# Kernel optimization log

Hardware: AMD Instinct MI355X
Metric: run time of the kernel (lower is better)

Reference implementation:

```python
import jax, jax.numpy as jnp
import numpy as np
from jax import lax

NPOINTS = 1024
K = 32
EPS = 1e-5


def fps(xyz, npoints):
    # Furthest point sampling. xyz: (B, N, 3) -> idx (B, npoints) int32.
    B, N, _ = xyz.shape
    def step(carry, _):
        dists, last = carry
        last_xyz = jnp.take_along_axis(xyz, last[:, None, None], axis=1)  # (B,1,3)
        d = jnp.sum((xyz - last_xyz) ** 2, axis=-1)  # (B,N)
        dists = jnp.minimum(dists, d)
        nxt = jnp.argmax(dists, axis=-1).astype(jnp.int32)
        return (dists, nxt), last
    init = (jnp.full((B, N), 1e10, xyz.dtype), jnp.zeros((B,), jnp.int32))
    _, idx = lax.scan(step, init, None, length=npoints)
    return idx.T  # (B, npoints)


def knn_idx(new_xyz, xyz, k):
    # new_xyz (B,S,3), xyz (B,N,3) -> (B,S,k) indices of k nearest neighbors.
    d = (jnp.sum(new_xyz ** 2, -1)[:, :, None]
         - 2.0 * jnp.einsum('bsc,bnc->bsn', new_xyz, xyz)
         + jnp.sum(xyz ** 2, -1)[:, None, :])  # (B,S,N)
    _, idx = lax.top_k(-d, k)
    return idx


def batch_gather(x, idx):
    # x (B, N, C), idx (B, ...) -> (B, ..., C)
    return jax.vmap(lambda a, i: a[i])(x, idx)


def bn(x, g, b, axes):
    # training-mode batchnorm over `axes`, channel on last axis
    m = jnp.mean(x, axes, keepdims=True)
    v = jnp.var(x, axes, keepdims=True)
    return g * (x - m) * lax.rsqrt(v + EPS) + b


def setup_inputs() -> dict:
    key = jax.random.key(0)
    ks = jax.random.split(key, 8)
    B, N, D, Cw, OUT = 16, 4096, 64, 64, 64
    inp = {
        'xyz': jax.random.uniform(ks[0], (B, N, 3), jnp.float32),
        'feature': jax.random.normal(ks[1], (B, D, N), jnp.float32),
        'w0': jax.random.normal(ks[2], (3, Cw), jnp.float32) * 0.3,
        'b0': jnp.zeros((Cw,), jnp.float32),
        'g0': jnp.ones((Cw,), jnp.float32),
        'be0': jnp.zeros((Cw,), jnp.float32),
        'w1': jax.random.normal(ks[3], (Cw, Cw), jnp.float32) * 0.1,
        'b1': jnp.zeros((Cw,), jnp.float32),
        'g1': jnp.ones((Cw,), jnp.float32),
        'be1': jnp.zeros((Cw,), jnp.float32),
        'w2': jax.random.normal(ks[4], (Cw, Cw), jnp.float32) * 0.1,
        'b2': jnp.zeros((Cw,), jnp.float32),
        'g2': jnp.ones((Cw,), jnp.float32),
        'be2': jnp.zeros((Cw,), jnp.float32),
        'wf': jax.random.normal(ks[5], (D * Cw, OUT), jnp.float32) * 0.02,
        'bf': jnp.zeros((OUT,), jnp.float32),
        'gf': jnp.ones((OUT,), jnp.float32),
        'bef': jnp.zeros((OUT,), jnp.float32),
    }
    return inp


def reference(xyz, feature, w0, b0, g0, be0, w1, b1, g1, be1, w2, b2, g2, be2, wf, bf, gf, bef):
    B, N, _ = xyz.shape
    # FPS + gather centroids
    fps_idx = fps(xyz, NPOINTS)                    # (B, S)
    new_xyz = batch_gather(xyz, fps_idx)           # (B, S, 3)
    # kNN grouping
    idx = knn_idx(new_xyz, xyz, K)                 # (B, S, K)
    grouped_xyz = batch_gather(xyz, idx) - new_xyz[:, :, None, :]   # (B,S,K,3)
    feat_nlast = jnp.swapaxes(feature, 1, 2)       # (B, N, D)
    grouped_feature = batch_gather(feat_nlast, idx)  # (B, S, K, D)
    # WeightNet: 1x1 conv MLP 3 -> Cw -> Cw -> Cw with BN+ReLU
    h = grouped_xyz
    for w, b, g, be in ((w0, b0, g0, be0), (w1, b1, g1, be1), (w2, b2, g2, be2)):
        h = jax.nn.relu(bn(h @ w + b, g, be, (0, 1, 2)))  # (B,S,K,Cw)
    weights = h
    # per-centroid matmul: (B,S,D,K) x (B,S,K,Cw) -> (B,S,D,Cw)
    nf = jnp.einsum('bskd,bskw->bsdw', grouped_feature, weights)
    nf = nf.reshape(B, NPOINTS, -1)                # (B, S, D*Cw)
    # final Conv1d(1x1) + BN1d + ReLU
    out = jax.nn.relu(bn(nf @ wf + bf, gf, bef, (0, 1)))  # (B, S, OUT)
    out = jnp.swapaxes(out, 1, 2)                  # (B, OUT, S)
    return (new_xyz, out)
```

## Files before the change

kernel.cpp:

```cpp
#include <hip/hip_runtime.h>

#define NBATCH 16
#define NPTS   4096
#define NSAMP  1024
#define NKNN   32
#define NROWS  (NBATCH*NSAMP*NKNN)
#define BN_EPS 1e-5f
#define H1PAD  66
#define KNN_CAP 512

typedef __attribute__((ext_vector_type(4))) float f32x4;
typedef __attribute__((ext_vector_type(8))) short bf16x8;
union frag_u { unsigned u[4]; bf16x8 h; uint4 u4; };

__device__ __forceinline__ unsigned pack_bf16pair(float a, float b) {
    unsigned ua = __float_as_uint(a); ua += 0x7FFFu + ((ua >> 16) & 1u);
    unsigned ub = __float_as_uint(b); ub += 0x7FFFu + ((ub >> 16) & 1u);
    return (ua >> 16) | (ub & 0xFFFF0000u);
}
__device__ __forceinline__ unsigned short bf16_rne(float a) {
    unsigned ua = __float_as_uint(a); ua += 0x7FFFu + ((ua >> 16) & 1u);
    return (unsigned short)(ua >> 16);
}

__global__ __launch_bounds__(256) void fps_kernel(const float* __restrict__ xyz,
                                                  float* __restrict__ newxyz)
{
    const int b = blockIdx.x;
    const int tid = threadIdx.x;
    const int wv = tid >> 6;
    const float* xb = xyz + (size_t)b * NPTS * 3;
    __shared__ float xs[NPTS];
    __shared__ float ys[NPTS];
    __shared__ float zs[NPTS];
    __shared__ __align__(16) float4 red[2][4];
    __shared__ __align__(16) float nxs[NSAMP*3];
    float px[16], py[16], pz[16], dmin[16];
    {
        float arr[48];
        const float4* s4 = (const float4*)(xb + (size_t)tid * 48);
        #pragma unroll
        for (int i = 0; i < 12; ++i) *(float4*)&arr[i*4] = s4[i];
        #pragma unroll
        for (int j = 0; j < 16; ++j) {
            px[j] = arr[3*j]; py[j] = arr[3*j+1]; pz[j] = arr[3*j+2];
            const int p = tid * 16 + j;
            xs[p] = px[j]; ys[p] = py[j]; zs[p] = pz[j];
            dmin[j] = 1e10f;
        }
    }
    if (tid == 0) { nxs[0] = xb[0]; nxs[1] = xb[1]; nxs[2] = xb[2]; }
    __syncthreads();
    float lx = xs[0], ly = ys[0], lz = zs[0];
    for (int t = 1; t < NSAMP; ++t) {
        float bv = -1.0f;
        #pragma unroll
        for (int j = 0; j < 16; ++j) {
            const float dx = __fsub_rn(px[j], lx);
            const float dy = __fsub_rn(py[j], ly);
            const float dz = __fsub_rn(pz[j], lz);
            const float d = __fadd_rn(__fadd_rn(__fmul_rn(dx,dx), __fmul_rn(dy,dy)), __fmul_rn(dz,dz));
            const float nd = fminf(dmin[j], d);
            dmin[j] = nd;
            bv = fmaxf(bv, nd);
        }
        int lj = 0;
        #pragma unroll
        for (int j = 15; j >= 0; --j) if (dmin[j] == bv) lj = j;
        const int bi_lane = tid * 16 + lj;
        float mv = bv;
        {
            int s_;
            s_ = __builtin_amdgcn_mov_dpp(__float_as_int(mv), 0x111, 0xf, 0xf, true);
            mv = fmaxf(mv, __int_as_float(s_));
            s_ = __builtin_amdgcn_mov_dpp(__float_as_int(mv), 0x112, 0xf, 0xf, true);
            mv = fmaxf(mv, __int_as_float(s_));
            s_ = __builtin_amdgcn_mov_dpp(__float_as_int(mv), 0x114, 0xf, 0xf, true);
            mv = fmaxf(mv, __int_as_float(s_));
            s_ = __builtin_amdgcn_mov_dpp(__float_as_int(mv), 0x118, 0xf, 0xf, true);
            mv = fmaxf(mv, __int_as_float(s_));
            s_ = __builtin_amdgcn_mov_dpp(__float_as_int(mv), 0x142, 0xf, 0xf, true);
            mv = fmaxf(mv, __int_as_float(s_));
            s_ = __builtin_amdgcn_mov_dpp(__float_as_int(mv), 0x143, 0xf, 0xf, true);
            mv = fmaxf(mv, __int_as_float(s_));
        }
        mv = __int_as_float(__builtin_amdgcn_readlane(__float_as_int(mv), 63));
        const unsigned long long mask = __ballot(bv == mv);
        const int winner = __ffsll(mask) - 1;
        const int bi_w = __builtin_amdgcn_readlane(bi_lane, winner);
        const float wx = xs[bi_w], wy = ys[bi_w], wz = zs[bi_w];
        const int par = t & 1;
        if ((tid & 63) == 0) red[par][wv] = make_float4(mv, wx, wy, wz);
        __syncthreads();
        float4 w0 = red[par][0];
        const float4 w1 = red[par][1];
        const float4 w2 = red[par][2];
        const float4 w3 = red[par][3];
        if (w1.x > w0.x) w0 = w1;
        if (w2.x > w0.x) w0 = w2;
        if (w3.x > w0.x) w0 = w3;
        lx = w0.y; ly = w0.z; lz = w0.w;
        if (tid == 0) { nxs[t*3] = lx; nxs[t*3+1] = ly; nxs[t*3+2] = lz; }
    }
    __syncthreads();
    {
        float4* d4 = (float4*)(newxyz + (size_t)b * NSAMP * 3);
        const float4* s4 = (const float4*)nxs;
        #pragma unroll
        for (int i = tid; i < NSAMP*3/4; i += 256) d4[i] = s4[i];
    }
}

__device__ __forceinline__ void bin_select(int* hist, int* ctrl, int* wsum,
                                           int tid, int shift)
{
    const int lane = tid & 63, wv = tid >> 6;
    const int cnt = hist[tid];
    const int r = ctrl[1];
    int incl = cnt;
    #pragma unroll
    for (int d = 1; d < 64; d <<= 1) {
        const int v = __shfl_up(incl, d);
        if (lane >= d) incl += v;
    }
    if (lane == 63) wsum[wv] = incl;
    __syncthreads();
    int base = 0;
    if (wv > 0) base += wsum[0];
    if (wv > 1) base += wsum[1];
    if (wv > 2) base += wsum[2];
    incl += base;
    const int excl = incl - cnt;
    if (excl < r && r <= incl) {
        ctrl[0] |= tid << shift;
        ctrl[1] = r - excl;
        ctrl[2] = cnt;
    }
}

__global__ __launch_bounds__(256) void knn_kernel(const float* __restrict__ xyz,
                                                  const float* __restrict__ newxyz,
                                                  int* __restrict__ idx_out)
{
    const int bs = blockIdx.x;
    const int b = bs >> 10;
    const int tid = threadIdx.x;
    const int lane = tid & 63;
    __shared__ unsigned keys[NPTS];
    __shared__ int hist[256];
    __shared__ float qsh[3];
    __shared__ int ctrl[8];
    __shared__ int wsum[4];
    __shared__ int cl[KNN_CAP];
    __shared__ int lt[32];
    __shared__ int ties[128];
    if (tid < 3) qsh[tid] = newxyz[bs*3 + tid];
    if (tid == 0) { ctrl[0] = 0; ctrl[1] = NKNN; }
    hist[tid] = 0;
    __syncthreads();
    const float q0 = qsh[0], q1 = qsh[1], q2 = qsh[2];
    const float qq = __fadd_rn(__fadd_rn(__fmul_rn(q0,q0), __fmul_rn(q1,q1)), __fmul_rn(q2,q2));
    const float* xb = xyz + (size_t)b * NPTS * 3;
    for (int n = tid; n < NPTS; n += 256) {
        const float x0 = xb[n*3+0], x1 = xb[n*3+1], x2 = xb[n*3+2];
        const float xx = __fadd_rn(__fadd_rn(__fmul_rn(x0,x0), __fmul_rn(x1,x1)), __fmul_rn(x2,x2));
        float dt = __fmul_rn(q0, x0);
        dt = __fmaf_rn(q1, x1, dt);
        dt = __fmaf_rn(q2, x2, dt);
        const float dd = __fadd_rn(__fsub_rn(qq, __fmul_rn(2.0f, dt)), xx);
        unsigned ub = __float_as_uint(dd);
        ub = (ub & 0x80000000u) ? ~ub : (ub | 0x80000000u);
        keys[n] = ub;
        const int bin = (int)(ub >> 24);
        unsigned long long act = __ballot(true);
        while (act) {
            const int leader = __ffsll(act) - 1;
            const int lbin = __builtin_amdgcn_readlane(bin, leader);
            const unsigned long long same = __ballot(bin == lbin);
            if (lane == leader) atomicAdd(&hist[lbin], (int)__popcll(same));
            act &= ~same;
        }
    }
    __syncthreads();
    bin_select(hist, ctrl, wsum, tid, 24);
    __syncthreads();
    const unsigned pf3 = (unsigned)ctrl[0];
    const int bin3 = (int)(pf3 >> 24);
    const int m = ctrl[2];
    const bool compact = (m <= KNN_CAP);
    if (tid == 0) { ctrl[3] = 0; ctrl[4] = 0; ctrl[5] = 0; ctrl[6] = 0; }
    __syncthreads();
    if (compact) {
        for (int n = tid; n < NPTS; n += 256) {
            const int tb = (int)(keys[n] >> 24);
            if (tb == bin3)      { const int pos = atomicAdd(&ctrl[3], 1); cl[pos] = n; }
            else if (tb < bin3)  { const int pos = atomicAdd(&ctrl[4], 1); lt[pos] = n; }
        }
    }
    __syncthreads();
    for (int p = 2; p >= 0; --p) {
        hist[tid] = 0;
        __syncthreads();
        const unsigned pre = (unsigned)ctrl[0];
        const int shift = p * 8;
        const unsigned himask = 0xFFFFFFFFu << ((p + 1) * 8);
        if (compact) {
            const int eqn = ctrl[3];
            for (int i = tid; i < eqn; i += 256) {
                const unsigned k = keys[cl[i]];
                if ((k & himask) == pre) atomicAdd(&hist[(k >> shift) & 255], 1);
            }
        } else {
            for (int n = tid; n < NPTS; n += 256) {
                const unsigned k = keys[n];
                if ((k & himask) == pre) atomicAdd(&hist[(k >> shift) & 255], 1);
            }
        }
        __syncthreads();
        bin_select(hist, ctrl, wsum, tid, shift);
        __syncthreads();
    }
    const unsigned T = (unsigned)ctrl[0];
    int* out = idx_out + (size_t)bs * NKNN;
    if (compact) {
        const int ltn = ctrl[4];
        if (tid == 0) ctrl[5] = ltn;
        __syncthreads();
        if (tid < ltn) out[tid] = lt[tid];
        const int eqn = ctrl[3];
        for (int i = tid; i < eqn; i += 256) {
            const int n = cl[i];
            const unsigned k = keys[n];
            if (k < T) {
                const int pos = atomicAdd(&ctrl[5], 1);
                if (pos < NKNN) out[pos] = n;
            } else if (k == T) {
                const int pos = atomicAdd(&ctrl[6], 1);
                if (pos < 128) ties[pos] = n;
            }
        }
    } else {
        for (int n = tid; n < NPTS; n += 256) {
            const unsigned k = keys[n];
            if (k < T) {
                const int pos = atomicAdd(&ctrl[5], 1);
                if (pos < NKNN) out[pos] = n;
            } else if (k == T) {
                const int pos = atomicAdd(&ctrl[6], 1);
                if (pos < 128) ties[pos] = n;
            }
        }
    }
    __syncthreads();
    if (tid == 0) {
        const int nless = ctrl[5] < NKNN ? ctrl[5] : NKNN;
        const int need = NKNN - nless;
        const int ntie = ctrl[6] < 128 ? ctrl[6] : 128;
        int last = -1;
        for (int j = 0; j < need; ++j) {
            int best = 0x7fffffff;
            for (int i = 0; i < ntie; ++i) {
                const int v = ties[i];
                if (v > last && v < best) best = v;
            }
            out[nless + j] = (best == 0x7fffffff) ? 0 : best;
            last = best;
        }
    }
}

__global__ __launch_bounds__(256) void feat_transpose_kernel(
    const float* __restrict__ feat, unsigned short* __restrict__ tfeat)
{
    __shared__ unsigned short t[64][65];
    const int blk = blockIdx.x;
    const int b = blk >> 6, nt = blk & 63;
    const int tid = threadIdx.x;
    #pragma unroll
    for (int i = 0; i < 16; ++i) {
        const int e = i*256 + tid;
        const int d = e >> 6, n = e & 63;
        t[n][d] = bf16_rne(feat[((size_t)(b*64 + d))*NPTS + nt*64 + n]);
    }
    __syncthreads();
    #pragma unroll
    for (int i = 0; i < 16; ++i) {
        const int e = i*256 + tid;
        const int n = e >> 6, d = e & 63;
        tfeat[((size_t)(b*NPTS) + nt*64 + n)*64 + d] = t[n][d];
    }
}

__global__ void zero_all_kernel(double* st, float* g1, float* g2)
{
    const int i = blockIdx.x * 256 + threadIdx.x;
    if (i < 512) st[i] = 0.0;
    if (i < 4096) { g1[i] = 0.f; g2[i] = 0.f; }
}

__global__ __launch_bounds__(256) void gxmoments_kernel(
    const float* __restrict__ xyz, const float* __restrict__ newxyz,
    const int* __restrict__ idxws, double* __restrict__ stats,
    float* __restrict__ gxws)
{
    const int tid = threadIdx.x;
    float m[9];
    #pragma unroll
    for (int i = 0; i < 9; ++i) m[i] = 0.f;
    for (int row = blockIdx.x * 256 + tid; row < NROWS; row += gridDim.x * 256) {
        const int bs = row >> 5;
        const int bb = row >> 15;
        const int id = idxws[row];
        const float* xp = xyz + ((size_t)bb * NPTS + id) * 3;
        const float* qp = newxyz + bs * 3;
        const float dx = xp[0] - qp[0];
        const float dy = xp[1] - qp[1];
        const float dz = xp[2] - qp[2];
        gxws[(size_t)row*3 + 0] = dx;
        gxws[(size_t)row*3 + 1] = dy;
        gxws[(size_t)row*3 + 2] = dz;
        m[0] += dx; m[1] += dy; m[2] += dz;
        m[3] += dx*dx; m[4] += dx*dy; m[5] += dx*dz;
        m[6] += dy*dy; m[7] += dy*dz; m[8] += dz*dz;
    }
    double d[9];
    #pragma unroll
    for (int i = 0; i < 9; ++i) {
        d[i] = (double)m[i];
        #pragma unroll
        for (int s = 1; s < 64; s <<= 1) d[i] += __shfl_xor(d[i], s);
    }
    __shared__ double part[4][9];
    if ((tid & 63) == 0) {
        #pragma unroll
        for (int i = 0; i < 9; ++i) part[tid >> 6][i] = d[i];
    }
    __syncthreads();
    if (tid < 9) atomicAdd(&stats[tid], part[0][tid] + part[1][tid] + part[2][tid] + part[3][tid]);
}

__global__ void bn0_moments_finalize_kernel(const double* __restrict__ st,
    const float* __restrict__ w0, const float* __restrict__ b0,
    const float* __restrict__ g0, const float* __restrict__ be0,
    float* __restrict__ outp)
{
    const int c = threadIdx.x;
    const double N = (double)NROWS;
    const double w0c = w0[c], w1c = w0[64 + c], w2c = w0[128 + c];
    const double b = b0[c];
    const double dotS = st[0]*w0c + st[1]*w1c + st[2]*w2c;
    const double qf = w0c*w0c*st[3] + w1c*w1c*st[6] + w2c*w2c*st[8]
                    + 2.0*(w0c*w1c*st[4] + w0c*w2c*st[5] + w1c*w2c*st[7]);
    const double mean = dotS / N + b;
    const double ex2 = (qf + 2.0*b*dotS) / N + b*b;
    const double var = ex2 - mean*mean;
    const float scale = g0[c] * rsqrtf((float)var + BN_EPS);
    outp[c] = scale;
    outp[64 + c] = be0[c] - (float)mean * scale;
}

__global__ void wfpack_all_kernel(const float* __restrict__ wf,
                                  const float* __restrict__ w1,
                                  const float* __restrict__ w2,
                                  unsigned* __restrict__ wfb,
                                  unsigned* __restrict__ w1b,
                                  unsigned* __restrict__ w2b)
{
    int blk = blockIdx.x;
    const float* src; unsigned* dst;
    if (blk < 512)      { src = wf; dst = wfb; }
    else if (blk < 520) { src = w1; dst = w1b; blk -= 512; }
    else                { src = w2; dst = w2b; blk -= 520; }
    const int kt = blk >> 2, ot = blk & 3;
    const int l = threadIdx.x;
    const int o = ot*16 + (l & 15);
    const int kb = kt*32 + (l >> 4)*8;
    unsigned out[4];
    #pragma unroll
    for (int r = 0; r < 4; ++r) {
        const float a = src[(size_t)(kb + 2*r) * 64 + o];
        const float b = src[(size_t)(kb + 2*r + 1) * 64 + o];
        out[r] = pack_bf16pair(a, b);
    }
    *(uint4*)&dst[((size_t)blk * 64 + l) * 4] = *(const uint4*)out;
}

__global__ __launch_bounds__(256) void gram1_kernel(
    const float* __restrict__ gxws,
    const float* __restrict__ w0, const float* __restrict__ b0,
    const float* __restrict__ bnp, float* __restrict__ G1,
    double* __restrict__ Sh1)
{
    __shared__ float gxs[32][3];
    __shared__ float h1s[32][H1PAD];
    __shared__ float rsum[256];
    const int tid = threadIdx.x;
    const int c = tid & 63;
    const int rq = tid >> 6;
    const int lg = c >> 4, lm = c & 15;
    const float w0c0 = w0[c], w0c1 = w0[64+c], w0c2 = w0[128+c];
    const float b0c = b0[c], sc0 = bnp[c], sh0 = bnp[64+c];
    f32x4 Ga[4] = {{0,0,0,0},{0,0,0,0},{0,0,0,0},{0,0,0,0}};
    float sumh = 0.f;
    for (int chunk = blockIdx.x; chunk < NROWS/32; chunk += gridDim.x) {
        if (tid < 96) ((float*)gxs)[tid] = gxws[(size_t)chunk*96 + tid];
        __syncthreads();
        #pragma unroll
        for (int i = 0; i < 8; ++i) {
            const int r = rq*8 + i;
            const float t0 = gxs[r][0]*w0c0 + gxs[r][1]*w0c1 + gxs[r][2]*w0c2 + b0c;
            const float h = fmaxf(sc0*t0 + sh0, 0.f);
            h1s[r][c] = h;
            sumh += h;
        }
        __syncthreads();
        frag_u fr[4];
        #pragma unroll
        for (int ct = 0; ct < 4; ++ct)
            #pragma unroll
            for (int r = 0; r < 4; ++r)
                fr[ct].u[r] = pack_bf16pair(h1s[lg*8 + 2*r][ct*16 + lm],
                                            h1s[lg*8 + 2*r + 1][ct*16 + lm]);
        #pragma unroll
        for (int ct = 0; ct < 4; ++ct)
            Ga[ct] = __builtin_amdgcn_mfma_f32_16x16x32_bf16(fr[rq].h, fr[ct].h, Ga[ct], 0, 0, 0);
        __syncthreads();
    }
    #pragma unroll
    for (int ct = 0; ct < 4; ++ct)
        #pragma unroll
        for (int r = 0; r < 4; ++r)
            atomicAdd(&G1[(rq*16 + lg*4 + r)*64 + ct*16 + lm], Ga[ct][r]);
    rsum[tid] = sumh;
    __syncthreads();
    if (tid < 64) atomicAdd(&Sh1[c], (double)(rsum[c] + rsum[64+c] + rsum[128+c] + rsum[192+c]));
}

__global__ __launch_bounds__(256) void gram2_kernel(
    const float* __restrict__ gxws,
    const float* __restrict__ w0, const float* __restrict__ b0,
    const float* __restrict__ b1, const unsigned* __restrict__ w1b,
    const float* __restrict__ bnp, float* __restrict__ G2,
    double* __restrict__ Sh2)
{
    __shared__ float gxs[32][3];
    __shared__ float h1s[32][H1PAD];
    __shared__ float h2s[32][H1PAD];
    __shared__ float rsum[256];
    const int tid = threadIdx.x;
    const int c = tid & 63;
    const int rq = tid >> 6;
    const int lg = c >> 4, lm = c & 15;
    const int c2 = rq*16 + lm;
    const float w0c0 = w0[c], w0c1 = w0[64+c], w0c2 = w0[128+c];
    const float b0c = b0[c], sc0 = bnp[c], sh0 = bnp[64+c];
    const float b1c2 = b1[c2], sc1 = bnp[128+c2], sh1 = bnp[192+c2];
    frag_u Bw1[2];
    Bw1[0].u4 = *(const uint4*)&w1b[((0*4 + rq)*64 + c)*4];
    Bw1[1].u4 = *(const uint4*)&w1b[((1*4 + rq)*64 + c)*4];
    f32x4 Ga[4] = {{0,0,0,0},{0,0,0,0},{0,0,0,0},{0,0,0,0}};
    float sumh = 0.f;
    for (int chunk = blockIdx.x; chunk < NROWS/32; chunk += gridDim.x) {
        if (tid < 96) ((float*)gxs)[tid] = gxws[(size_t)chunk*96 + tid];
        __syncthreads();
        #pragma unroll
        for (int i = 0; i < 8; ++i) {
            const int r = rq*8 + i;
            const float t0 = gxs[r][0]*w0c0 + gxs[r][1]*w0c1 + gxs[r][2]*w0c2 + b0c;
            h1s[r][c] = fmaxf(sc0*t0 + sh0, 0.f);
        }
        __syncthreads();
        #pragma unroll
        for (int mt = 0; mt < 2; ++mt) {
            f32x4 acc = {0,0,0,0};
            #pragma unroll
            for (int kt = 0; kt < 2; ++kt) {
                frag_u a;
                #pragma unroll
                for (int r = 0; r < 4; ++r) {
                    const float2 f = *(const float2*)&h1s[mt*16 + lm][kt*32 + lg*8 + 2*r];
                    a.u[r] = pack_bf16pair(f.x, f.y);
                }
                acc = __builtin_amdgcn_mfma_f32_16x16x32_bf16(a.h, Bw1[kt].h, acc, 0, 0, 0);
            }
            #pragma unroll
            for (int r = 0; r < 4; ++r)
                h2s[mt*16 + lg*4 + r][c2] = fmaxf(sc1*(acc[r] + b1c2) + sh1, 0.f);
        }
        __syncthreads();
        #pragma unroll
        for (int i = 0; i < 8; ++i) sumh += h2s[rq*8 + i][c];
        frag_u fr[4];
        #pragma unroll
        for (int ct = 0; ct < 4; ++ct)
            #pragma unroll
            for (int r = 0; r < 4; ++r)
                fr[ct].u[r] = pack_bf16pair(h2s[lg*8 + 2*r][ct*16 + lm],
                                            h2s[lg*8 + 2*r + 1][ct*16 + lm]);
        #pragma unroll
        for (int ct = 0; ct < 4; ++ct)
            Ga[ct] = __builtin_amdgcn_mfma_f32_16x16x32_bf16(fr[rq].h, fr[ct].h, Ga[ct], 0, 0, 0);
        __syncthreads();
    }
    #pragma unroll
    for (int ct = 0; ct < 4; ++ct)
        #pragma unroll
        for (int r = 0; r < 4; ++r)
            atomicAdd(&G2[(rq*16 + lg*4 + r)*64 + ct*16 + lm], Ga[ct][r]);
    rsum[tid] = sumh;
    __syncthreads();
    if (tid < 64) atomicAdd(&Sh2[c], (double)(rsum[c] + rsum[64+c] + rsum[128+c] + rsum[192+c]));
}

__global__ __launch_bounds__(256) void bn_gram_finalize_kernel(
    const double* __restrict__ Sh, const float* __restrict__ G,
    const float* __restrict__ w, const float* __restrict__ bias,
    const float* __restrict__ g, const float* __restrict__ be,
    float* __restrict__ outp)
{
    __shared__ float wls[64][65];
    __shared__ double shl[64];
    __shared__ double rd[256], rqd[256];
    const int tid = threadIdx.x;
    const int c = tid & 63;
    const int rqi = tid >> 6;
    for (int i = tid; i < 4096; i += 256) wls[i >> 6][i & 63] = w[i];
    if (tid < 64) shl[tid] = Sh[tid];
    __syncthreads();
    double dot = 0.0, quad = 0.0;
    for (int j = rqi*16; j < rqi*16 + 16; ++j) {
        const double wjc = (double)wls[j][c];
        dot += wjc * shl[j];
        double inner = 0.0;
        for (int k = 0; k < 64; ++k) inner += (double)G[j*64 + k] * (double)wls[k][c];
        quad += wjc * inner;
    }
    rd[tid] = dot; rqd[tid] = quad;
    __syncthreads();
    if (tid < 64) {
        const double d = rd[c] + rd[64+c] + rd[128+c] + rd[192+c];
        const double q = rqd[c] + rqd[64+c] + rqd[128+c] + rqd[192+c];
        const double N = (double)NROWS;
        const double bc = (double)bias[c];
        const double mean = d / N + bc;
        const double ex2 = (q + 2.0*bc*d) / N + bc*bc;
        const double var = ex2 - mean*mean;
        const float scale = g[c] * rsqrtf((float)var + BN_EPS);
        outp[c] = scale;
        outp[64 + c] = be[c] - (float)mean * scale;
    }
}

__global__ void bn_finalize_kernel(const double* __restrict__ st,
                                   const float* __restrict__ g,
                                   const float* __restrict__ be,
                                   float* __restrict__ outp, float n)
{
    const int c = threadIdx.x;
    const double m = st[c] / (double)n;
    const double var = st[64 + c] / (double)n - m * m;
    const float scale = g[c] * rsqrtf((float)var + BN_EPS);
    outp[c] = scale;
    outp[64 + c] = be[c] - (float)m * scale;
}

__global__ __launch_bounds__(256) void final_conv_kernel(
    const float* __restrict__ gxws,
    const int* __restrict__ idxws, const unsigned short* __restrict__ tfeat,
    const float* __restrict__ w0, const float* __restrict__ b0,
    const float* __restrict__ b1, const float* __restrict__ b2,
    const float* __restrict__ bnp, const unsigned* __restrict__ wfb,
    const unsigned* __restrict__ w1b, const unsigned* __restrict__ w2b,
    const float* __restrict__ bf, float* __restrict__ y)
{
    __shared__ unsigned wtp[8][16][64];
    __shared__ __align__(16) float scratch[2*64*H1PAD];
    __shared__ float gxs[256][3];
    __shared__ int   idxs[8][32];
    float* h1s = scratch;
    float* h2s = scratch + 64*H1PAD;
    unsigned* yaf = (unsigned*)scratch;
    const int tid = threadIdx.x;
    const int c = tid & 63;
    const int rq = tid >> 6;
    const int lg = c >> 4, lm = c & 15;
    const int c2 = rq*16 + lm;
    const int bs0 = blockIdx.x * 8;
    const int b = bs0 >> 10;
    idxs[tid >> 5][tid & 31] = idxws[(size_t)bs0 * NKNN + tid];
    const float w0c0 = w0[c], w0c1 = w0[64+c], w0c2 = w0[128+c];
    const float b0c = b0[c], sc0 = bnp[c], sh0 = bnp[64+c];
    const float b1c2 = b1[c2], sc1 = bnp[128+c2], sh1 = bnp[192+c2];
    const float b2c2 = b2[c2], sc2 = bnp[256+c2], sh2 = bnp[320+c2];
    frag_u Bw1[2], Bw2[2];
    #pragma unroll
    for (int kt = 0; kt < 2; ++kt) {
        Bw1[kt].u4 = *(const uint4*)&w1b[((kt*4 + rq)*64 + c)*4];
        Bw2[kt].u4 = *(const uint4*)&w2b[((kt*4 + rq)*64 + c)*4];
    }
    for (int i = tid; i < 768; i += 256)
        ((float*)gxs)[i] = gxws[(size_t)bs0*96 + i];
    __syncthreads();
    for (int chunk = 0; chunk < 4; ++chunk) {
        #pragma unroll
        for (int i = 0; i < 16; ++i) {
            const int r = rq*16 + i;
            const int gr = chunk*64 + r;
            const float t0 = gxs[gr][0]*w0c0 + gxs[gr][1]*w0c1 + gxs[gr][2]*w0c2 + b0c;
            h1s[r*H1PAD + c] = fmaxf(sc0*t0 + sh0, 0.f);
        }
        __syncthreads();
        #pragma unroll
        for (int mt = 0; mt < 4; ++mt) {
            f32x4 acc = {0,0,0,0};
            #pragma unroll
            for (int kt = 0; kt < 2; ++kt) {
                frag_u a;
                #pragma unroll
                for (int r = 0; r < 4; ++r) {
                    const float2 f = *(const float2*)&h1s[(mt*16 + lm)*H1PAD + kt*32 + lg*8 + 2*r];
                    a.u[r] = pack_bf16pair(f.x, f.y);
                }
                acc = __builtin_amdgcn_mfma_f32_16x16x32_bf16(a.h, Bw1[kt].h, acc, 0, 0, 0);
            }
            #pragma unroll
            for (int r = 0; r < 4; ++r)
                h2s[(mt*16 + lg*4 + r)*H1PAD + c2] = fmaxf(sc1*(acc[r] + b1c2) + sh1, 0.f);
        }
        __syncthreads();
        #pragma unroll
        for (int mt = 0; mt < 4; ++mt) {
            f32x4 acc = {0,0,0,0};
            #pragma unroll
            for (int kt = 0; kt < 2; ++kt) {
                frag_u a;
                #pragma unroll
                for (int r = 0; r < 4; ++r) {
                    const float2 f = *(const float2*)&h2s[(mt*16 + lm)*H1PAD + kt*32 + lg*8 + 2*r];
                    a.u[r] = pack_bf16pair(f.x, f.y);
                }
                acc = __builtin_amdgcn_mfma_f32_16x16x32_bf16(a.h, Bw2[kt].h, acc, 0, 0, 0);
            }
            float wt[4];
            #pragma unroll
            for (int r = 0; r < 4; ++r)
                wt[r] = fmaxf(sc2*(acc[r] + b2c2) + sh2, 0.f);
            const int grow0 = chunk*64 + mt*16 + lg*4;
            const int e = grow0 >> 5, kl = grow0 & 31;
            wtp[e][kl >> 1][c2]       = pack_bf16pair(wt[0], wt[1]);
            wtp[e][(kl >> 1) + 1][c2] = pack_bf16pair(wt[2], wt[3]);
        }
        __syncthreads();
    }
    const int lane = c;
    const int wid = rq;
    frag_u afr[2][4];
    #pragma unroll
    for (int es = 0; es < 2; ++es)
        #pragma unroll
        for (int w4 = 0; w4 < 4; ++w4)
            #pragma unroll
            for (int r = 0; r < 4; ++r)
                afr[es][w4].u[r] = wtp[wid*2 + es][lg*4 + r][w4*16 + lm];
    f32x4 yaccA = {0.f, 0.f, 0.f, 0.f};
    f32x4 yaccB = {0.f, 0.f, 0.f, 0.f};
    const unsigned short* tfb = tfeat + (size_t)b * NPTS * 64;
    for (int dhalf = 0; dhalf < 2; ++dhalf) {
        #pragma unroll
        for (int es = 0; es < 2; ++es) {
            const int e = wid*2 + es;
            #pragma unroll
            for (int dt = 0; dt < 2; ++dt) {
                const int d = dhalf*32 + dt*16 + lm;
                frag_u B;
                #pragma unroll
                for (int r = 0; r < 4; ++r) {
                    const int k0 = lg*8 + 2*r;
                    const unsigned va = tfb[(size_t)idxs[e][k0]   * 64 + d];
                    const unsigned vb = tfb[(size_t)idxs[e][k0+1] * 64 + d];
                    B.u[r] = va | (vb << 16);
                }
                #pragma unroll
                for (int w4 = 0; w4 < 4; ++w4) {
                    f32x4 dnf = {0.f, 0.f, 0.f, 0.f};
                    dnf = __builtin_amdgcn_mfma_f32_16x16x32_bf16(afr[es][w4].h, B.h, dnf, 0, 0, 0);
                    const unsigned p0 = pack_bf16pair(dnf[0], dnf[1]);
                    const unsigned p1 = pack_bf16pair(dnf[2], dnf[3]);
                    const int dloc = dt*16 + lm;
                    const int kp0 = dloc*32 + w4*8 + lg*2;
                    const int sw = kp0 ^ ((lm & 3) << 3) ^ ((e & 7) << 2);
                    *(uint2*)&yaf[e*1024 + sw] = make_uint2(p0, p1);
                }
            }
        }
        __syncthreads();
        for (int kt = 0; kt < 64; kt += 2) {
            frag_u A0, B0, A1, B1;
            const int kpb0 = (kt*16 + lg*4) ^ (((kt >> 1) & 3) << 3) ^ ((lm & 7) << 2);
            const int kpb1 = ((kt+1)*16 + lg*4) ^ ((((kt+1) >> 1) & 3) << 3) ^ ((lm & 7) << 2);
            A0.u4 = *(const uint4*)&yaf[(lm & 7)*1024 + kpb0];
            A1.u4 = *(const uint4*)&yaf[(lm & 7)*1024 + kpb1];
            B0.u4 = *(const uint4*)&wfb[(((size_t)(dhalf*64 + kt)*4 + wid)*64 + lane)*4];
            B1.u4 = *(const uint4*)&wfb[(((size_t)(dhalf*64 + kt + 1)*4 + wid)*64 + lane)*4];
            yaccA = __builtin_amdgcn_mfma_f32_16x16x32_bf16(A0.h, B0.h, yaccA, 0, 0, 0);
            yaccB = __builtin_amdgcn_mfma_f32_16x16x32_bf16(A1.h, B1.h, yaccB, 0, 0, 0);
        }
        __syncthreads();
    }
    if (lg < 2) {
        const float bfo = bf[wid*16 + lm];
        #pragma unroll
        for (int r = 0; r < 4; ++r)
            y[(size_t)(bs0 + lg*4 + r) * 64 + wid*16 + lm] = (yaccA[r] + yaccB[r]) + bfo;
    }
}

__global__ __launch_bounds__(256) void ystats_kernel(const float* __restrict__ y,
                                                     double* __restrict__ st)
{
    const int tid = threadIdx.x;
    const int c = tid & 63;
    double s = 0.0, s2 = 0.0;
    for (int i = blockIdx.x * 256 + tid; i < NBATCH*NSAMP*64; i += gridDim.x * 256) {
        const float v = y[i];
        s += v; s2 += (double)v * (double)v;
    }
    __shared__ double rs[256], rs2[256];
    rs[tid] = s; rs2[tid] = s2;
    __syncthreads();
    if (tid < 64) {
        const double a  = rs[c]  + rs[64+c]  + rs[128+c]  + rs[192+c];
        const double a2 = rs2[c] + rs2[64+c] + rs2[128+c] + rs2[192+c];
        atomicAdd(&st[c], a);
        atomicAdd(&st[64 + c], a2);
    }
}

__global__ void writeout_kernel(const float* __restrict__ y,
                                const float* __restrict__ bnp3,
                                float* __restrict__ outp)
{
    const int i = blockIdx.x * 256 + threadIdx.x;
    if (i >= NBATCH * 64 * NSAMP) return;
    const int s = i & 1023;
    const int o = (i >> 10) & 63;
    const int bb = i >> 16;
    const float v = y[((size_t)(bb << 10) + s) * 64 + o];
    outp[i] = fmaxf(bnp3[o] * v + bnp3[64 + o], 0.f);
}

extern "C" void kernel_launch(void* const* d_in, const int* in_sizes, int n_in,
                              void* d_out, int out_size, void* d_ws, size_t ws_size,
                              hipStream_t stream)
{
    (void)in_sizes; (void)n_in; (void)out_size; (void)ws_size;
    const float* xyz  = (const float*)d_in[0];
    const float* feat = (const float*)d_in[1];
    const float* w0   = (const float*)d_in[2];
    const float* b0   = (const float*)d_in[3];
    const float* g0   = (const float*)d_in[4];
    const float* be0  = (const float*)d_in[5];
    const float* w1   = (const float*)d_in[6];
    const float* b1   = (const float*)d_in[7];
    const float* g1   = (const float*)d_in[8];
    const float* be1  = (const float*)d_in[9];
    const float* w2   = (const float*)d_in[10];
    const float* b2   = (const float*)d_in[11];
    const float* g2   = (const float*)d_in[12];
    const float* be2  = (const float*)d_in[13];
    const float* wf   = (const float*)d_in[14];
    const float* bf   = (const float*)d_in[15];
    const float* gf   = (const float*)d_in[16];
    const float* bef  = (const float*)d_in[17];

    float* out = (float*)d_out;
    float* newxyz = out;
    float* outmain = out + NBATCH * NSAMP * 3;

    char* ws = (char*)d_ws;
    int*      idxws = (int*)ws;
    float*    ybuf  = (float*)(ws + 2097152);
    double*   stats = (double*)(ws + 6291456);
    float*    bnp   = (float*)(ws + 6295552);
    unsigned* wfb   = (unsigned*)(ws + 6297600);
    unsigned* w1b   = (unsigned*)(ws + 6821888);
    unsigned* w2b   = (unsigned*)(ws + 6830080);
    float*    G1    = (float*)(ws + 6838272);
    float*    G2    = (float*)(ws + 6854656);
    float*    gxws  = (float*)(ws + 6871040);
    unsigned short* tfeat = (unsigned short*)(ws + 13164544);

    zero_all_kernel<<<16, 256, 0, stream>>>(stats, G1, G2);
    wfpack_all_kernel<<<528, 64, 0, stream>>>(wf, w1, w2, wfb, w1b, w2b);
    feat_transpose_kernel<<<1024, 256, 0, stream>>>(feat, tfeat);
    fps_kernel<<<NBATCH, 256, 0, stream>>>(xyz, newxyz);
    knn_kernel<<<NBATCH * NSAMP, 256, 0, stream>>>(xyz, newxyz, idxws);

    gxmoments_kernel<<<1024, 256, 0, stream>>>(xyz, newxyz, idxws, stats, gxws);
    bn0_moments_finalize_kernel<<<1, 64, 0, stream>>>(stats, w0, b0, g0, be0, bnp);
    gram1_kernel<<<256, 256, 0, stream>>>(gxws, w0, b0, bnp, G1, stats + 128);
    bn_gram_finalize_kernel<<<1, 256, 0, stream>>>(stats + 128, G1, w1, b1, g1, be1, bnp + 128);
    gram2_kernel<<<256, 256, 0, stream>>>(gxws, w0, b0, b1, w1b, bnp, G2, stats + 192);
    bn_gram_finalize_kernel<<<1, 256, 0, stream>>>(stats + 192, G2, w2, b2, g2, be2, bnp + 256);

    final_conv_kernel<<<NBATCH * NSAMP / 8, 256, 0, stream>>>(
        gxws, idxws, tfeat, w0, b0, b1, b2, bnp, wfb, w1b, w2b, bf, ybuf);

    ystats_kernel<<<256, 256, 0, stream>>>(ybuf, stats + 384);
    bn_finalize_kernel<<<1, 64, 0, stream>>>(stats + 384, gf, bef, bnp + 384, (float)(NBATCH * NSAMP));
    writeout_kernel<<<4096, 256, 0, stream>>>(ybuf, bnp + 384, outmain);
}
```

Measured before the change: 1.236 ms.

## Merge FPS, transpose, weight packing and zeroing into one prep launch; fuse grouped-xyz into kNN

The zero, weight-pack and feature-transpose kernels are folded into the FPS launch as extra blocks, sharing LDS through a union. The aim is to overlap the serial 16-block FPS with the independent prep work and to cut launch count. The kNN kernel now stages its indices in LDS and writes the centered neighbour coordinates itself, so gxmoments only reads gxws instead of gathering. The risk is that the larger LDS footprint of the merged kernel limits occupancy for the transpose blocks.

```diff
diff --git a/kernel.cpp b/kernel.cpp
--- a/kernel.cpp
+++ b/kernel.cpp
@@ -23,18 +23,74 @@
     return (unsigned short)(ua >> 16);
 }
 
-__global__ __launch_bounds__(256) void fps_kernel(const float* __restrict__ xyz,
-                                                  float* __restrict__ newxyz)
-{
-    const int b = blockIdx.x;
+union PrepLds {
+    struct {
+        float xs[NPTS]; float ys[NPTS]; float zs[NPTS];
+        float4 red[2][4];
+        float nxs[NSAMP*3];
+    } f;
+    unsigned short tt[64][65];
+};
+
+__global__ __launch_bounds__(256) void prep_kernel(
+    const float* __restrict__ xyz, float* __restrict__ newxyz,
+    const float* __restrict__ feat, unsigned short* __restrict__ tfeat,
+    const float* __restrict__ wf, const float* __restrict__ w1,
+    const float* __restrict__ w2, unsigned* __restrict__ wfb,
+    unsigned* __restrict__ w1b, unsigned* __restrict__ w2b,
+    double* __restrict__ st, float* __restrict__ g1f, float* __restrict__ g2f)
+{
+    __shared__ PrepLds L;
+    const int blk = blockIdx.x;
     const int tid = threadIdx.x;
+    if (blk >= 1172) {
+        const int i = (blk - 1172) * 256 + tid;
+        if (i < 512) st[i] = 0.0;
+        if (i < 4096) { g1f[i] = 0.f; g2f[i] = 0.f; }
+        return;
+    }
+    if (blk >= 1040) {
+        const int unit = (blk - 1040) * 4 + (tid >> 6);
+        const int l = tid & 63;
+        int u = unit;
+        const float* src; unsigned* dst;
+        if (u < 512)      { src = wf; dst = wfb; }
+        else if (u < 520) { src = w1; dst = w1b; u -= 512; }
+        else              { src = w2; dst = w2b; u -= 520; }
+        const int kt = u >> 2, ot = u & 3;
+        const int o = ot*16 + (l & 15);
+        const int kb = kt*32 + (l >> 4)*8;
+        unsigned outp[4];
+        #pragma unroll
+        for (int r = 0; r < 4; ++r) {
+            const float a = src[(size_t)(kb + 2*r) * 64 + o];
+            const float b = src[(size_t)(kb + 2*r + 1) * 64 + o];
+            outp[r] = pack_bf16pair(a, b);
+        }
+        *(uint4*)&dst[((size_t)u * 64 + l) * 4] = *(const uint4*)outp;
+        return;
+    }
+    if (blk >= 16) {
+        const int t = blk - 16;
+        const int b = t >> 6, nt = t & 63;
+        #pragma unroll
+        for (int i = 0; i < 16; ++i) {
+            const int e = i*256 + tid;
+            const int d = e >> 6, n = e & 63;
+            L.tt[n][d] = bf16_rne(feat[((size_t)(b*64 + d))*NPTS + nt*64 + n]);
+        }
+        __syncthreads();
+        #pragma unroll
+        for (int i = 0; i < 16; ++i) {
+            const int e = i*256 + tid;
+            const int n = e >> 6, d = e & 63;
+            tfeat[((size_t)(b*NPTS) + nt*64 + n)*64 + d] = L.tt[n][d];
+        }
+        return;
+    }
+    const int b = blk;
     const int wv = tid >> 6;
     const float* xb = xyz + (size_t)b * NPTS * 3;
-    __shared__ float xs[NPTS];
-    __shared__ float ys[NPTS];
-    __shared__ float zs[NPTS];
-    __shared__ __align__(16) float4 red[2][4];
-    __shared__ __align__(16) float nxs[NSAMP*3];
     float px[16], py[16], pz[16], dmin[16];
     {
         float arr[48];
@@ -45,13 +101,13 @@
         for (int j = 0; j < 16; ++j) {
             px[j] = arr[3*j]; py[j] = arr[3*j+1]; pz[j] = arr[3*j+2];
             const int p = tid * 16 + j;
-            xs[p] = px[j]; ys[p] = py[j]; zs[p] = pz[j];
+            L.f.xs[p] = px[j]; L.f.ys[p] = py[j]; L.f.zs[p] = pz[j];
             dmin[j] = 1e10f;
         }
     }
-    if (tid == 0) { nxs[0] = xb[0]; nxs[1] = xb[1]; nxs[2] = xb[2]; }
-    __syncthreads();
-    float lx = xs[0], ly = ys[0], lz = zs[0];
+    if (tid == 0) { L.f.nxs[0] = xb[0]; L.f.nxs[1] = xb[1]; L.f.nxs[2] = xb[2]; }
+    __syncthreads();
+    float lx = L.f.xs[0], ly = L.f.ys[0], lz = L.f.zs[0];
     for (int t = 1; t < NSAMP; ++t) {
         float bv = -1.0f;
         #pragma unroll
@@ -88,24 +144,24 @@
         const unsigned long long mask = __ballot(bv == mv);
         const int winner = __ffsll(mask) - 1;
         const int bi_w = __builtin_amdgcn_readlane(bi_lane, winner);
-        const float wx = xs[bi_w], wy = ys[bi_w], wz = zs[bi_w];
+        const float wx = L.f.xs[bi_w], wy = L.f.ys[bi_w], wz = L.f.zs[bi_w];
         const int par = t & 1;
-        if ((tid & 63) == 0) red[par][wv] = make_float4(mv, wx, wy, wz);
-        __syncthreads();
-        float4 w0 = red[par][0];
-        const float4 w1 = red[par][1];
-        const float4 w2 = red[par][2];
-        const float4 w3 = red[par][3];
-        if (w1.x > w0.x) w0 = w1;
-        if (w2.x > w0.x) w0 = w2;
-        if (w3.x > w0.x) w0 = w3;
+        if ((tid & 63) == 0) L.f.red[par][wv] = make_float4(mv, wx, wy, wz);
+        __syncthreads();
+        float4 w0 = L.f.red[par][0];
+        const float4 w1v = L.f.red[par][1];
+        const float4 w2v = L.f.red[par][2];
+        const float4 w3v = L.f.red[par][3];
+        if (w1v.x > w0.x) w0 = w1v;
+        if (w2v.x > w0.x) w0 = w2v;
+        if (w3v.x > w0.x) w0 = w3v;
         lx = w0.y; ly = w0.z; lz = w0.w;
-        if (tid == 0) { nxs[t*3] = lx; nxs[t*3+1] = ly; nxs[t*3+2] = lz; }
+        if (tid == 0) { L.f.nxs[t*3] = lx; L.f.nxs[t*3+1] = ly; L.f.nxs[t*3+2] = lz; }
     }
     __syncthreads();
     {
         float4* d4 = (float4*)(newxyz + (size_t)b * NSAMP * 3);
-        const float4* s4 = (const float4*)nxs;
+        const float4* s4 = (const float4*)L.f.nxs;
         #pragma unroll
         for (int i = tid; i < NSAMP*3/4; i += 256) d4[i] = s4[i];
     }
@@ -140,7 +196,8 @@
 
 __global__ __launch_bounds__(256) void knn_kernel(const float* __restrict__ xyz,
                                                   const float* __restrict__ newxyz,
-                                                  int* __restrict__ idx_out)
+                                                  int* __restrict__ idx_out,
+                                                  float* __restrict__ gxws)
 {
     const int bs = blockIdx.x;
     const int b = bs >> 10;
@@ -154,6 +211,7 @@
     __shared__ int cl[KNN_CAP];
     __shared__ int lt[32];
     __shared__ int ties[128];
+    __shared__ int outl[NKNN];
     if (tid < 3) qsh[tid] = newxyz[bs*3 + tid];
     if (tid == 0) { ctrl[0] = 0; ctrl[1] = NKNN; }
     hist[tid] = 0;
@@ -221,19 +279,18 @@
         __syncthreads();
     }
     const unsigned T = (unsigned)ctrl[0];
-    int* out = idx_out + (size_t)bs * NKNN;
     if (compact) {
         const int ltn = ctrl[4];
         if (tid == 0) ctrl[5] = ltn;
         __syncthreads();
-        if (tid < ltn) out[tid] = lt[tid];
+        if (tid < ltn) outl[tid] = lt[tid];
         const int eqn = ctrl[3];
         for (int i = tid; i < eqn; i += 256) {
             const int n = cl[i];
             const unsigned k = keys[n];
             if (k < T) {
                 const int pos = atomicAdd(&ctrl[5], 1);
-                if (pos < NKNN) out[pos] = n;
+                if (pos < NKNN) outl[pos] = n;
             } else if (k == T) {
                 const int pos = atomicAdd(&ctrl[6], 1);
                 if (pos < 128) ties[pos] = n;
@@ -244,7 +301,7 @@
             const unsigned k = keys[n];
             if (k < T) {
                 const int pos = atomicAdd(&ctrl[5], 1);
-                if (pos < NKNN) out[pos] = n;
+                if (pos < NKNN) outl[pos] = n;
             } else if (k == T) {
                 const int pos = atomicAdd(&ctrl[6], 1);
                 if (pos < 128) ties[pos] = n;
@@ -263,62 +320,29 @@
                 const int v = ties[i];
                 if (v > last && v < best) best = v;
             }
-            out[nless + j] = (best == 0x7fffffff) ? 0 : best;
+            outl[nless + j] = (best == 0x7fffffff) ? 0 : best;
             last = best;
         }
     }
-}
-
-__global__ __launch_bounds__(256) void feat_transpose_kernel(
-    const float* __restrict__ feat, unsigned short* __restrict__ tfeat)
-{
-    __shared__ unsigned short t[64][65];
-    const int blk = blockIdx.x;
-    const int b = blk >> 6, nt = blk & 63;
-    const int tid = threadIdx.x;
-    #pragma unroll
-    for (int i = 0; i < 16; ++i) {
-        const int e = i*256 + tid;
-        const int d = e >> 6, n = e & 63;
-        t[n][d] = bf16_rne(feat[((size_t)(b*64 + d))*NPTS + nt*64 + n]);
-    }
-    __syncthreads();
-    #pragma unroll
-    for (int i = 0; i < 16; ++i) {
-        const int e = i*256 + tid;
-        const int n = e >> 6, d = e & 63;
-        tfeat[((size_t)(b*NPTS) + nt*64 + n)*64 + d] = t[n][d];
-    }
-}
-
-__global__ void zero_all_kernel(double* st, float* g1, float* g2)
-{
-    const int i = blockIdx.x * 256 + threadIdx.x;
-    if (i < 512) st[i] = 0.0;
-    if (i < 4096) { g1[i] = 0.f; g2[i] = 0.f; }
+    __syncthreads();
+    if (tid < NKNN) idx_out[(size_t)bs * NKNN + tid] = outl[tid];
+    if (tid < 96) {
+        const int k = tid / 3, cc = tid % 3;
+        gxws[((size_t)bs * NKNN + k) * 3 + cc] = xb[outl[k]*3 + cc] - qsh[cc];
+    }
 }
 
 __global__ __launch_bounds__(256) void gxmoments_kernel(
-    const float* __restrict__ xyz, const float* __restrict__ newxyz,
-    const int* __restrict__ idxws, double* __restrict__ stats,
-    float* __restrict__ gxws)
+    const float* __restrict__ gxws, double* __restrict__ stats)
 {
     const int tid = threadIdx.x;
     float m[9];
     #pragma unroll
     for (int i = 0; i < 9; ++i) m[i] = 0.f;
     for (int row = blockIdx.x * 256 + tid; row < NROWS; row += gridDim.x * 256) {
-        const int bs = row >> 5;
-        const int bb = row >> 15;
-        const int id = idxws[row];
-        const float* xp = xyz + ((size_t)bb * NPTS + id) * 3;
-        const float* qp = newxyz + bs * 3;
-        const float dx = xp[0] - qp[0];
-        const float dy = xp[1] - qp[1];
-        const float dz = xp[2] - qp[2];
-        gxws[(size_t)row*3 + 0] = dx;
-        gxws[(size_t)row*3 + 1] = dy;
-        gxws[(size_t)row*3 + 2] = dz;
+        const float dx = gxws[(size_t)row*3 + 0];
+        const float dy = gxws[(size_t)row*3 + 1];
+        const float dz = gxws[(size_t)row*3 + 2];
         m[0] += dx; m[1] += dy; m[2] += dz;
         m[3] += dx*dx; m[4] += dx*dy; m[5] += dx*dz;
         m[6] += dy*dy; m[7] += dy*dz; m[8] += dz*dz;
@@ -357,32 +381,6 @@
     const float scale = g0[c] * rsqrtf((float)var + BN_EPS);
     outp[c] = scale;
     outp[64 + c] = be0[c] - (float)mean * scale;
-}
-
-__global__ void wfpack_all_kernel(const float* __restrict__ wf,
-                                  const float* __restrict__ w1,
-                                  const float* __restrict__ w2,
-                                  unsigned* __restrict__ wfb,
-                                  unsigned* __restrict__ w1b,
-                                  unsigned* __restrict__ w2b)
-{
-    int blk = blockIdx.x;
-    const float* src; unsigned* dst;
-    if (blk < 512)      { src = wf; dst = wfb; }
-    else if (blk < 520) { src = w1; dst = w1b; blk -= 512; }
-    else                { src = w2; dst = w2b; blk -= 520; }
-    const int kt = blk >> 2, ot = blk & 3;
-    const int l = threadIdx.x;
-    const int o = ot*16 + (l & 15);
-    const int kb = kt*32 + (l >> 4)*8;
-    unsigned out[4];
-    #pragma unroll
-    for (int r = 0; r < 4; ++r) {
-        const float a = src[(size_t)(kb + 2*r) * 64 + o];
-        const float b = src[(size_t)(kb + 2*r + 1) * 64 + o];
-        out[r] = pack_bf16pair(a, b);
-    }
-    *(uint4*)&dst[((size_t)blk * 64 + l) * 4] = *(const uint4*)out;
 }
 
 __global__ __launch_bounds__(256) void gram1_kernel(
@@ -790,13 +788,12 @@
     float*    gxws  = (float*)(ws + 6871040);
     unsigned short* tfeat = (unsigned short*)(ws + 13164544);
 
-    zero_all_kernel<<<16, 256, 0, stream>>>(stats, G1, G2);
-    wfpack_all_kernel<<<528, 64, 0, stream>>>(wf, w1, w2, wfb, w1b, w2b);
-    feat_transpose_kernel<<<1024, 256, 0, stream>>>(feat, tfeat);
-    fps_kernel<<<NBATCH, 256, 0, stream>>>(xyz, newxyz);
-    knn_kernel<<<NBATCH * NSAMP, 256, 0, stream>>>(xyz, newxyz, idxws);
-
-    gxmoments_kernel<<<1024, 256, 0, stream>>>(xyz, newxyz, idxws, stats, gxws);
+    prep_kernel<<<1188, 256, 0, stream>>>(xyz, newxyz, feat, tfeat,
+                                          wf, w1, w2, wfb, w1b, w2b,
+                                          stats, G1, G2);
+    knn_kernel<<<NBATCH * NSAMP, 256, 0, stream>>>(xyz, newxyz, idxws, gxws);
+
+    gxmoments_kernel<<<1024, 256, 0, stream>>>(gxws, stats);
     bn0_moments_finalize_kernel<<<1, 64, 0, stream>>>(stats, w0, b0, g0, be0, bnp);
     gram1_kernel<<<256, 256, 0, stream>>>(gxws, w0, b0, bnp, G1, stats + 128);
     bn_gram_finalize_kernel<<<1, 256, 0, stream>>>(stats + 128, G1, w1, b1, g1, be1, bnp + 128);
```

New measurement: 1.231 ms. No clear change (-0.4%).
